# Optimization experiments

Measured on AMD Instinct MI355X. Metric: run time of the kernel, lower is better.

The kernel has to match this reference:

```python
import jax, jax.numpy as jnp
import numpy as np

IN_C, OUT_C, SCALE, S, NF = 2, 2, 2, 3, 64
MODES = 3
NB = IN_C * MODES  # one sub-module per (input channel, mode)
PAD = S - 1


def _pixel_shuffle(x, r):
    n, c, h, w = x.shape
    oc = c // (r * r)
    x = x.reshape(n, oc, r, r, h, w).transpose(0, 1, 4, 2, 5, 3)
    return x.reshape(n, oc, h * r, w * r)


def _round_ste(x):
    # straight-through round: forward = round(x), backward = identity
    return x + jax.lax.stop_gradient(jnp.round(x) - x)


def _branch(xin, w1, b1, w2, b2, w3, b3, w4, b4, w5, b5, w6, b6):
    # xin: [4B, 2, H+PAD, W+PAD]; tiny SxS conv then dense 1x1 chain (MuLUT unit)
    y = jax.lax.conv_general_dilated(xin, w1, (1, 1), 'VALID',
                                     dimension_numbers=('NCHW', 'OIHW', 'NCHW'))
    y = jax.nn.relu(y + b1[None, :, None, None])

    def dense(t, w, b):
        f = jax.nn.relu(jnp.einsum('bchw,oc->bohw', t, w) + b[None, :, None, None])
        return jnp.concatenate([t, f], axis=1)

    y = dense(y, w2, b2)
    y = dense(y, w3, b3)
    y = dense(y, w4, b4)
    y = dense(y, w5, b5)
    return jnp.einsum('bchw,oc->bohw', y, w6) + b6[None, :, None, None]


def _forward(x, prev_x, W1, B1, W2, B2, W3, B3, W4, B4, W5, B5, W6, B6):
    B, _, H, W = x.shape

    def prep(c):
        # rotating x and prev_x jointly == rotating each separately (elementwise pairing preserved)
        xc = jnp.concatenate([x[:, c:c + 1], prev_x[:, c:c + 1]], axis=1)  # [B,2,H,W]
        rs = jnp.concatenate([jnp.rot90(xc, k=r, axes=(2, 3)) for r in range(4)], axis=0)  # [4B,2,H,W]
        return jnp.pad(rs, ((0, 0), (0, 0), (0, PAD), (0, PAD)), mode='edge')  # replicate pad right/bottom

    xs = jnp.stack([prep(c) for c in range(IN_C)])           # [IN_C,4B,2,Hp,Wp]
    xb = xs[np.repeat(np.arange(IN_C), MODES)]               # [NB,4B,2,Hp,Wp]
    y = jax.vmap(_branch)(xb, W1, B1, W2, B2, W3, B3, W4, B4, W5, B5, W6, B6)  # [NB,4B,OC*sc^2,H,W]
    y = jax.vmap(lambda t: _pixel_shuffle(t, SCALE))(y)      # [NB,4B,OC,sH,sW]
    y = y.reshape(NB, 4, B, OUT_C, SCALE * H, SCALE * W)
    y = jnp.stack([jnp.rot90(y[:, r], k=(4 - r) % 4, axes=(3, 4)) for r in range(4)], axis=1)
    y = _round_ste(jnp.tanh(y) * 127.0)
    # sum over rotations and modes per channel, then over channels; divide by in_c (output_quant=False)
    return y.sum(axis=(0, 1)) / IN_C


def setup_inputs():
    key = jax.random.key(0)
    ks = jax.random.split(key, 8)
    B, H = 2, 64

    def w(k, shape, fan_in):
        return jax.random.normal(k, shape, jnp.float32) * np.float32(np.sqrt(2.0 / fan_in))

    return {
        'x': jax.random.uniform(ks[0], (B, IN_C, H, H), jnp.float32),
        'prev_x': jax.random.uniform(ks[1], (B, IN_C, H, H), jnp.float32),
        'W1': w(ks[2], (NB, NF, 2, S, S), 2 * S * S), 'B1': jnp.zeros((NB, NF), jnp.float32),
        'W2': w(ks[3], (NB, NF, NF), NF), 'B2': jnp.zeros((NB, NF), jnp.float32),
        'W3': w(ks[4], (NB, NF, 2 * NF), 2 * NF), 'B3': jnp.zeros((NB, NF), jnp.float32),
        'W4': w(ks[5], (NB, NF, 3 * NF), 3 * NF), 'B4': jnp.zeros((NB, NF), jnp.float32),
        'W5': w(ks[6], (NB, NF, 4 * NF), 4 * NF), 'B5': jnp.zeros((NB, NF), jnp.float32),
        'W6': w(ks[7], (NB, OUT_C * SCALE * SCALE, 5 * NF), 5 * NF),
        'B6': jnp.zeros((NB, OUT_C * SCALE * SCALE), jnp.float32),
    }


def reference(x, prev_x, W1, B1, W2, B2, W3, B3, W4, B4, W5, B5, W6, B6):
    return _forward(x, prev_x, W1, B1, W2, B2, W3, B3, W4, B4, W5, B5, W6, B6)
```

## Files before the change

### kernel.cpp

```cpp
#include <hip/hip_runtime.h>
#include <math.h>


typedef short bf16x8 __attribute__((ext_vector_type(8)));
typedef short short4v __attribute__((ext_vector_type(4)));
typedef float f32x4  __attribute__((ext_vector_type(4)));

__device__ __forceinline__ short f2bf_bits(float v) {
    union { float f; unsigned u; } x; x.f = v;
    unsigned r = x.u + 0x7FFFu + ((x.u >> 16) & 1u);
    return (short)(r >> 16);
}
__device__ __forceinline__ float bf2f(short s) {
    union { unsigned u; float f; } x; x.u = ((unsigned)(unsigned short)s) << 16;
    return x.f;
}

__global__ void prep_weights(const float* __restrict__ W1, const float* __restrict__ W2,
                             const float* __restrict__ W3, const float* __restrict__ W4,
                             const float* __restrict__ W5, const float* __restrict__ W6,
                             short* __restrict__ wsw, float* __restrict__ w1p,
                             float* __restrict__ outz)
{
    if (blockIdx.x < 135) {
        const int t = blockIdx.x * 256 + threadIdx.x;
        const int frag = t >> 6, lane = t & 63;
        const int b = frag / 90, slot = frag % 90;
        const int kqh = lane >> 4, rowl = lane & 15;
        const float* src; int K, kb, m; bool head = false;
        if (slot < 8)       { src = W2; K = 64;  kb = slot >> 2;        m = slot & 3; }
        else if (slot < 24) { src = W3; K = 128; kb = (slot - 8) >> 2;  m = slot & 3; }
        else if (slot < 48) { src = W4; K = 192; kb = (slot - 24) >> 2; m = slot & 3; }
        else if (slot < 80) { src = W5; K = 256; kb = (slot - 48) >> 2; m = slot & 3; }
        else                { src = W6; K = 320; kb = slot - 80; m = 0; head = true; }
        short* hi = wsw + (size_t)b * 92160 + slot * 1024 + (lane << 3);
        short* lo = hi + 512;
        #pragma unroll
        for (int j = 0; j < 8; ++j) {
            const int k = kb * 32 + ((j & 4) ? 16 : 0) + kqh * 4 + (j & 3);
            float v;
            if (!head) v = src[(size_t)(b * 64 + m * 16 + rowl) * K + k];
            else       v = (rowl < 8) ? src[(size_t)(b * 8 + rowl) * 320 + k] : 0.0f;
            const short h = f2bf_bits(v);
            hi[j] = h;
            lo[j] = f2bf_bits(v - bf2f(h));
        }
    } else if (blockIdx.x == 135) {
        for (int d = threadIdx.x; d < 6912; d += 256) {
            const int bq = d / 288, rem = d % 288;
            const int it2 = rem >> 4, s16 = (rem >> 2) & 3, tt = rem & 3;
            const int b = bq >> 2, kq = bq & 3;
            const int img = it2 / 9, tap = it2 % 9;
            w1p[d] = W1[(size_t)((b * 64 + s16 * 16 + kq * 4 + tt) * 2 + img) * 9 + tap];
        }
    } else {
        const int i = ((blockIdx.x - 136) * 256 + (int)threadIdx.x) * 8;
        f32x4 z = {0.f, 0.f, 0.f, 0.f};
        *(f32x4*)(outz + i)     = z;
        *(f32x4*)(outz + i + 4) = z;
    }
}

__device__ __forceinline__ void pack_kb(const f32x4 a, const f32x4 bq,
                                        bf16x8* ph, bf16x8* pl) {
    bf16x8 h, l;
    #pragma unroll
    for (int e = 0; e < 4; ++e) {
        float v = fmaxf(a[e], 0.0f);
        short hs = f2bf_bits(v);
        h[e] = hs; l[e] = f2bf_bits(v - bf2f(hs));
        float v2 = fmaxf(bq[e], 0.0f);
        short hs2 = f2bf_bits(v2);
        h[4 + e] = hs2; l[4 + e] = f2bf_bits(v2 - bf2f(hs2));
    }
    *ph = h; *pl = l;
}

__device__ __forceinline__ float sel4(int kq, const float* __restrict__ p) {
    const float b0 = p[0], b1 = p[4], b2 = p[8], b3 = p[12];
    const float lo = (kq & 1) ? b1 : b0;
    const float hi = (kq & 1) ? b3 : b2;
    return (kq & 2) ? hi : lo;
}

#define ASM_VMCNT(N) asm volatile("s_waitcnt vmcnt(" #N ")" ::: "memory")

#define DENSE_STAGE(KB_IN, SLOT0, BPTR, OUTKB)                                          \
  {                                                                                      \
    f32x4 sacc[4];                                                                       \
    _Pragma("unroll") for (int m = 0; m < 4; ++m)                                        \
      _Pragma("unroll") for (int rr = 0; rr < 4; ++rr) sacc[m][rr] = 0.f;                \
    _Pragma("unroll") for (int kb = 0; kb < KB_IN; ++kb) {                               \
      _Pragma("unroll") for (int m = 0; m < 4; ++m) {                                    \
        const int so = (SLOT0 + kb * 4 + m) * 1024 + lane8;                              \
        bf16x8 ah = *(const bf16x8*)&wlds[so];                                           \
        bf16x8 al = *(const bf16x8*)&wlds[so + 512];                                     \
        sacc[m] = __builtin_amdgcn_mfma_f32_16x16x32_bf16(ah, act_h[kb], sacc[m], 0, 0, 0); \
        sacc[m] = __builtin_amdgcn_mfma_f32_16x16x32_bf16(ah, act_l[kb], sacc[m], 0, 0, 0); \
        sacc[m] = __builtin_amdgcn_mfma_f32_16x16x32_bf16(al, act_h[kb], sacc[m], 0, 0, 0); \
      }                                                                                  \
    }                                                                                    \
    _Pragma("unroll") for (int m = 0; m < 4; ++m)                                        \
      _Pragma("unroll") for (int rr = 0; rr < 4; ++rr)                                   \
        sacc[m][rr] += sel4(kq, BPTR + m * 16 + rr);                                     \
    pack_kb(sacc[0], sacc[1], &act_h[OUTKB], &act_l[OUTKB]);                             \
    pack_kb(sacc[2], sacc[3], &act_h[OUTKB + 1], &act_l[OUTKB + 1]);                     \
  }

__global__ __launch_bounds__(1024) void mulut_main(
    const float* __restrict__ x, const float* __restrict__ px_,
    const float* __restrict__ B1, const float* __restrict__ B2,
    const float* __restrict__ B3, const float* __restrict__ B4,
    const float* __restrict__ B5, const float* __restrict__ B6,
    const short* __restrict__ wsw, const float* __restrict__ w1p,
    float* __restrict__ out)
{
    __shared__ short wlds[81920];

    const int blk = blockIdx.x;
    const int q   = blk & 15;
    const int n   = (blk >> 4) & 7;
    const int b   = blk >> 7;
    const int c   = (b >= 3) ? 1 : 0;
    const int r   = n >> 1;
    const int batch = n & 1;

    const int tid   = threadIdx.x;
    const int w     = tid >> 6;
    const int lane  = tid & 63;
    const int col   = lane & 15;
    const int kq    = lane >> 4;
    const int lane8 = lane << 3;

    const int row = q * 4 + (w >> 2);
    const int px  = (w & 3) * 16 + col;

    const char* wsb = (const char*)(wsw + (size_t)b * 92160);

    bf16x8 act_h[10];
    bf16x8 act_l[10];

    {
        const float* img0 = x   + ((batch * 2 + c) << 12);
        const float* img1 = px_ + ((batch * 2 + c) << 12);
        float g[2][9];
        #pragma unroll
        for (int di = 0; di < 3; ++di) {
            const int ii = min(row + di, 63);
            #pragma unroll
            for (int dj = 0; dj < 3; ++dj) {
                const int jj = min(px + dj, 63);
                int si, sj;
                if      (r == 0) { si = ii;      sj = jj;      }
                else if (r == 1) { si = jj;      sj = 63 - ii; }
                else if (r == 2) { si = 63 - ii; sj = 63 - jj; }
                else             { si = 63 - jj; sj = ii;      }
                g[0][di * 3 + dj] = img0[si * 64 + sj];
                g[1][di * 3 + dj] = img1[si * 64 + sj];
            }
        }

        f32x4 accc[4];
        #pragma unroll
        for (int s16 = 0; s16 < 4; ++s16)
            #pragma unroll
            for (int t = 0; t < 4; ++t) accc[s16][t] = 0.f;

        const f32x4* wp0 = (const f32x4*)&w1p[(b * 4 + kq) * 288];
        #pragma unroll
        for (int it = 0; it < 18; ++it) {
            const float gv = g[it / 9][it % 9];
            #pragma unroll
            for (int s16 = 0; s16 < 4; ++s16) {
                const f32x4 w4 = wp0[it * 4 + s16];
                #pragma unroll
                for (int t = 0; t < 4; ++t)
                    accc[s16][t] = fmaf(gv, w4[t], accc[s16][t]);
            }
        }
        #pragma unroll
        for (int m = 0; m < 4; ++m)
            #pragma unroll
            for (int rr = 0; rr < 4; ++rr)
                accc[m][rr] += sel4(kq, B1 + b * 64 + m * 16 + rr);
        pack_kb(accc[0], accc[1], &act_h[0], &act_l[0]);
        pack_kb(accc[2], accc[3], &act_h[1], &act_l[1]);
    }

    __builtin_amdgcn_sched_barrier(0);

    #pragma unroll
    for (int ck = 0; ck < 10; ++ck) {
        const unsigned off = ck * 16384 + w * 1024;
        __builtin_amdgcn_global_load_lds((const unsigned*)(wsb + off + lane * 16),
                                         (unsigned*)&wlds[off >> 1], 16, 0, 0);
    }
    __builtin_amdgcn_sched_barrier(0);

    ASM_VMCNT(9);
    __builtin_amdgcn_s_barrier();
    DENSE_STAGE(2, 0, B2 + b * 64, 2)

    ASM_VMCNT(7);
    __builtin_amdgcn_s_barrier();
    DENSE_STAGE(4, 8, B3 + b * 64, 4)

    __builtin_amdgcn_s_barrier();
    {
        const unsigned l0 = w * 1024;
        __builtin_amdgcn_global_load_lds((const unsigned*)(wsb + 163840 + l0 + lane * 16),
                                         (unsigned*)&wlds[l0 >> 1], 16, 0, 0);
        const unsigned l1 = 16384 + w * 256;
        __builtin_amdgcn_global_load_lds((const unsigned*)(wsb + 163840 + l1 + lane * 4),
                                         (unsigned*)&wlds[l1 >> 1], 4, 0, 0);
    }
    __builtin_amdgcn_sched_barrier(0);

    ASM_VMCNT(6);
    __builtin_amdgcn_s_barrier();
    DENSE_STAGE(6, 24, B4 + b * 64, 6)

    ASM_VMCNT(2);
    __builtin_amdgcn_s_barrier();
    DENSE_STAGE(8, 48, B5 + b * 64, 8)

    ASM_VMCNT(0);
    __builtin_amdgcn_s_barrier();

    f32x4 hacc;
    #pragma unroll
    for (int rr = 0; rr < 4; ++rr) hacc[rr] = 0.f;
    #pragma unroll
    for (int kb = 0; kb < 10; ++kb) {
        const int so = kb * 1024 + lane8;
        bf16x8 ah = *(const bf16x8*)&wlds[so];
        bf16x8 al = *(const bf16x8*)&wlds[so + 512];
        hacc = __builtin_amdgcn_mfma_f32_16x16x32_bf16(ah, act_h[kb], hacc, 0, 0, 0);
        hacc = __builtin_amdgcn_mfma_f32_16x16x32_bf16(ah, act_l[kb], hacc, 0, 0, 0);
        hacc = __builtin_amdgcn_mfma_f32_16x16x32_bf16(al, act_h[kb], hacc, 0, 0, 0);
    }
    #pragma unroll
    for (int rr = 0; rr < 4; ++rr) {
        const float h0 = B6[b * 8 + rr];
        const float h1 = B6[b * 8 + 4 + rr];
        hacc[rr] += (kq == 0) ? h0 : ((kq == 1) ? h1 : 0.f);
    }

    #pragma unroll
    for (int rr = 0; rr < 4; ++rr) {
        const int ch = kq * 4 + rr;
        if (ch < 8) {
            const int oc = ch >> 2;
            const int a  = (ch >> 1) & 1;
            const int bb = ch & 1;
            const int ip = 2 * row + a;
            const int jp = 2 * px + bb;
            int I, J;
            if      (r == 0) { I = ip;       J = jp;       }
            else if (r == 1) { I = jp;       J = 127 - ip; }
            else if (r == 2) { I = 127 - ip; J = 127 - jp; }
            else             { I = 127 - jp; J = ip;       }
            const float v = rintf(tanhf(hacc[rr]) * 127.0f);
            atomicAdd(out + (((batch * 2 + oc) << 14) + I * 128 + J), v * 0.5f);
        }
    }
}

extern "C" void kernel_launch(void* const* d_in, const int* in_sizes, int n_in,
                              void* d_out, int out_size, void* d_ws, size_t ws_size,
                              hipStream_t stream) {
    const float* x   = (const float*)d_in[0];
    const float* pxv = (const float*)d_in[1];
    const float* W1  = (const float*)d_in[2];
    const float* B1  = (const float*)d_in[3];
    const float* W2  = (const float*)d_in[4];
    const float* B2  = (const float*)d_in[5];
    const float* W3  = (const float*)d_in[6];
    const float* B3  = (const float*)d_in[7];
    const float* W4  = (const float*)d_in[8];
    const float* B4  = (const float*)d_in[9];
    const float* W5  = (const float*)d_in[10];
    const float* B5  = (const float*)d_in[11];
    const float* W6  = (const float*)d_in[12];
    const float* B6  = (const float*)d_in[13];
    float* out = (float*)d_out;

    short* wsw = (short*)d_ws;
    float* w1p = (float*)(wsw + 6 * 92160);

    prep_weights<<<dim3(168), dim3(256), 0, stream>>>(W1, W2, W3, W4, W5, W6,
                                                      wsw, w1p, out);
    mulut_main<<<dim3(768), dim3(1024), 0, stream>>>(
        x, pxv, B1, B2, B3, B4, B5, B6, wsw, w1p, out);
}
```

Baseline: 206.3 us.

## Double-buffer weight slots in smaller LDS, halve block size, stage weight prep via shared memory

The main kernel now uses 512-thread blocks with two rows per strip and a 64KB LDS split into two ping-pong buffers. Weight chunks stream in per stage and overlap with the MFMA work, which lets up to four blocks share a CU instead of one 160KB block. The prep kernel loads each weight matrix into shared memory with coalesced reads before swizzling, and writes vectorised bf16 hi/lo fragments using a padded per-branch stride. In exchange there are more barriers and more blocks, and each weight byte is reloaded from L2 by twice as many blocks.

```diff
diff --git a/kernel.cpp b/kernel.cpp
--- a/kernel.cpp
+++ b/kernel.cpp
@@ -3,8 +3,8 @@
 
 
 typedef short bf16x8 __attribute__((ext_vector_type(8)));
-typedef short short4v __attribute__((ext_vector_type(4)));
 typedef float f32x4  __attribute__((ext_vector_type(4)));
+typedef float f32x4g __attribute__((ext_vector_type(4)));
 
 __device__ __forceinline__ short f2bf_bits(float v) {
     union { float f; unsigned u; } x; x.f = v;
@@ -22,31 +22,49 @@
                              short* __restrict__ wsw, float* __restrict__ w1p,
                              float* __restrict__ outz)
 {
-    if (blockIdx.x < 135) {
-        const int t = blockIdx.x * 256 + threadIdx.x;
-        const int frag = t >> 6, lane = t & 63;
-        const int b = frag / 90, slot = frag % 90;
-        const int kqh = lane >> 4, rowl = lane & 15;
-        const float* src; int K, kb, m; bool head = false;
-        if (slot < 8)       { src = W2; K = 64;  kb = slot >> 2;        m = slot & 3; }
-        else if (slot < 24) { src = W3; K = 128; kb = (slot - 8) >> 2;  m = slot & 3; }
-        else if (slot < 48) { src = W4; K = 192; kb = (slot - 24) >> 2; m = slot & 3; }
-        else if (slot < 80) { src = W5; K = 256; kb = (slot - 48) >> 2; m = slot & 3; }
-        else                { src = W6; K = 320; kb = slot - 80; m = 0; head = true; }
-        short* hi = wsw + (size_t)b * 92160 + slot * 1024 + (lane << 3);
-        short* lo = hi + 512;
-        #pragma unroll
-        for (int j = 0; j < 8; ++j) {
-            const int k = kb * 32 + ((j & 4) ? 16 : 0) + kqh * 4 + (j & 3);
-            float v;
-            if (!head) v = src[(size_t)(b * 64 + m * 16 + rowl) * K + k];
-            else       v = (rowl < 8) ? src[(size_t)(b * 8 + rowl) * 320 + k] : 0.0f;
-            const short h = f2bf_bits(v);
-            hi[j] = h;
-            lo[j] = f2bf_bits(v - bf2f(h));
-        }
-    } else if (blockIdx.x == 135) {
-        for (int d = threadIdx.x; d < 6912; d += 256) {
+    __shared__ float S[16384];
+    const int blk = blockIdx.x, tid = threadIdx.x;
+
+    if (blk < 30) {
+        const int b = blk / 5, s = blk % 5;
+        const float* Wsrc[5] = { W2, W3, W4, W5, W6 };
+        const int rows = (s < 4) ? 64 : 8;
+        const int K    = 64 * (s + 1);
+        const int N    = rows * K;
+        const int slotbase[5] = { 0, 8, 24, 48, 80 };
+        const int nslots[5]   = { 8, 16, 24, 32, 12 };
+
+        const float* src = Wsrc[s] + (size_t)b * N;
+        for (int i = tid; i < (N >> 2); i += 256)
+            *(f32x4g*)&S[i << 2] = *(const f32x4g*)&src[i << 2];
+        __syncthreads();
+
+        const int NS = nslots[s];
+        for (int pp = tid; pp < NS * 64; pp += 256) {
+            const int l    = pp >> 6;
+            const int lane = pp & 63;
+            const int kb   = (s < 4) ? (l >> 2) : l;
+            const int m    = (s < 4) ? (l & 3) : 0;
+            const int rowl = lane & 15;
+            const int kqh  = lane >> 4;
+            bf16x8 hv, lv;
+            #pragma unroll
+            for (int j = 0; j < 8; ++j) {
+                const int k = kb * 32 + ((j & 4) ? 16 : 0) + kqh * 4 + (j & 3);
+                float v;
+                if (s < 4)                    v = S[(m * 16 + rowl) * K + k];
+                else if (rowl < 8 && l < 10)  v = S[rowl * 320 + k];
+                else                          v = 0.0f;
+                const short h = f2bf_bits(v);
+                hv[j] = h;
+                lv[j] = f2bf_bits(v - bf2f(h));
+            }
+            short* dst = wsw + (size_t)b * 94208 + (slotbase[s] + l) * 1024 + (lane << 3);
+            *(bf16x8*)dst         = hv;
+            *(bf16x8*)(dst + 512) = lv;
+        }
+    } else if (blk == 30) {
+        for (int d = tid; d < 6912; d += 256) {
             const int bq = d / 288, rem = d % 288;
             const int it2 = rem >> 4, s16 = (rem >> 2) & 3, tt = rem & 3;
             const int b = bq >> 2, kq = bq & 3;
@@ -54,10 +72,10 @@
             w1p[d] = W1[(size_t)((b * 64 + s16 * 16 + kq * 4 + tt) * 2 + img) * 9 + tap];
         }
     } else {
-        const int i = ((blockIdx.x - 136) * 256 + (int)threadIdx.x) * 8;
-        f32x4 z = {0.f, 0.f, 0.f, 0.f};
-        *(f32x4*)(outz + i)     = z;
-        *(f32x4*)(outz + i + 4) = z;
+        const int i = ((blk - 31) * 256 + tid) * 8;
+        f32x4g z = {0.f, 0.f, 0.f, 0.f};
+        *(f32x4g*)(outz + i)     = z;
+        *(f32x4g*)(outz + i + 4) = z;
     }
 }
 
@@ -84,30 +102,39 @@
 }
 
 #define ASM_VMCNT(N) asm volatile("s_waitcnt vmcnt(" #N ")" ::: "memory")
-
-#define DENSE_STAGE(KB_IN, SLOT0, BPTR, OUTKB)                                          \
-  {                                                                                      \
-    f32x4 sacc[4];                                                                       \
-    _Pragma("unroll") for (int m = 0; m < 4; ++m)                                        \
-      _Pragma("unroll") for (int rr = 0; rr < 4; ++rr) sacc[m][rr] = 0.f;                \
-    _Pragma("unroll") for (int kb = 0; kb < KB_IN; ++kb) {                               \
-      _Pragma("unroll") for (int m = 0; m < 4; ++m) {                                    \
-        const int so = (SLOT0 + kb * 4 + m) * 1024 + lane8;                              \
-        bf16x8 ah = *(const bf16x8*)&wlds[so];                                           \
-        bf16x8 al = *(const bf16x8*)&wlds[so + 512];                                     \
-        sacc[m] = __builtin_amdgcn_mfma_f32_16x16x32_bf16(ah, act_h[kb], sacc[m], 0, 0, 0); \
-        sacc[m] = __builtin_amdgcn_mfma_f32_16x16x32_bf16(ah, act_l[kb], sacc[m], 0, 0, 0); \
-        sacc[m] = __builtin_amdgcn_mfma_f32_16x16x32_bf16(al, act_h[kb], sacc[m], 0, 0, 0); \
-      }                                                                                  \
-    }                                                                                    \
-    _Pragma("unroll") for (int m = 0; m < 4; ++m)                                        \
-      _Pragma("unroll") for (int rr = 0; rr < 4; ++rr)                                   \
-        sacc[m][rr] += sel4(kq, BPTR + m * 16 + rr);                                     \
-    pack_kb(sacc[0], sacc[1], &act_h[OUTKB], &act_l[OUTKB]);                             \
-    pack_kb(sacc[2], sacc[3], &act_h[OUTKB + 1], &act_l[OUTKB + 1]);                     \
+#define MFMA(A, B, C) __builtin_amdgcn_mfma_f32_16x16x32_bf16(A, B, C, 0, 0, 0)
+
+#define ISSUE(SLOT0, NC, PB)                                                          \
+  _Pragma("unroll") for (int c = 0; c < NC; ++c) {                                    \
+    const unsigned lo_ = c * 8192u + w * 1024u;                                       \
+    __builtin_amdgcn_global_load_lds(                                                 \
+        (const unsigned*)(wsb + (SLOT0) * 2048 + lo_ + lane * 16),                    \
+        (unsigned*)&wlds[(PB) + (lo_ >> 1)], 16, 0, 0);                               \
   }
 
-__global__ __launch_bounds__(1024) void mulut_main(
+#define HALF(SACC, NKB, A0, PB, SLOT0)                                                \
+  _Pragma("unroll") for (int kb = 0; kb < NKB; ++kb)                                  \
+    _Pragma("unroll") for (int m = 0; m < 4; ++m) {                                   \
+      const int so = (PB) + ((SLOT0) + kb * 4 + m) * 1024 + lane8;                    \
+      bf16x8 ah = *(const bf16x8*)&wlds[so];                                          \
+      bf16x8 al = *(const bf16x8*)&wlds[so + 512];                                    \
+      SACC[m] = MFMA(ah, act_h[(A0) + kb], SACC[m]);                                  \
+      SACC[m] = MFMA(ah, act_l[(A0) + kb], SACC[m]);                                  \
+      SACC[m] = MFMA(al, act_h[(A0) + kb], SACC[m]);                                  \
+    }
+
+#define SACC_INIT(SACC)                                                               \
+  _Pragma("unroll") for (int m = 0; m < 4; ++m)                                       \
+    _Pragma("unroll") for (int rr = 0; rr < 4; ++rr) SACC[m][rr] = 0.f;
+
+#define FINISH(SACC, BPTR, OUTKB)                                                     \
+  _Pragma("unroll") for (int m = 0; m < 4; ++m)                                       \
+    _Pragma("unroll") for (int rr = 0; rr < 4; ++rr)                                  \
+      SACC[m][rr] += sel4(kq, (BPTR) + m * 16 + rr);                                  \
+  pack_kb(SACC[0], SACC[1], &act_h[OUTKB], &act_l[OUTKB]);                            \
+  pack_kb(SACC[2], SACC[3], &act_h[(OUTKB) + 1], &act_l[(OUTKB) + 1]);
+
+__global__ __launch_bounds__(512, 4) void mulut_main(
     const float* __restrict__ x, const float* __restrict__ px_,
     const float* __restrict__ B1, const float* __restrict__ B2,
     const float* __restrict__ B3, const float* __restrict__ B4,
@@ -115,14 +142,15 @@
     const short* __restrict__ wsw, const float* __restrict__ w1p,
     float* __restrict__ out)
 {
-    __shared__ short wlds[81920];
-
-    const int blk = blockIdx.x;
-    const int q   = blk & 15;
-    const int n   = (blk >> 4) & 7;
-    const int b   = blk >> 7;
-    const int c   = (b >= 3) ? 1 : 0;
-    const int r   = n >> 1;
+    __shared__ short wlds[32768];
+    const int P1 = 16384;
+
+    const int blk   = blockIdx.x;
+    const int strip = blk & 31;
+    const int n     = (blk >> 5) & 7;
+    const int b     = blk >> 8;
+    const int c     = (b >= 3) ? 1 : 0;
+    const int r     = n >> 1;
     const int batch = n & 1;
 
     const int tid   = threadIdx.x;
@@ -132,10 +160,10 @@
     const int kq    = lane >> 4;
     const int lane8 = lane << 3;
 
-    const int row = q * 4 + (w >> 2);
+    const int row = strip * 2 + (w >> 2);
     const int px  = (w & 3) * 16 + col;
 
-    const char* wsb = (const char*)(wsw + (size_t)b * 92160);
+    const char* wsb = (const char*)(wsw + (size_t)b * 94208);
 
     bf16x8 act_h[10];
     bf16x8 act_l[10];
@@ -159,13 +187,8 @@
                 g[1][di * 3 + dj] = img1[si * 64 + sj];
             }
         }
-
         f32x4 accc[4];
-        #pragma unroll
-        for (int s16 = 0; s16 < 4; ++s16)
-            #pragma unroll
-            for (int t = 0; t < 4; ++t) accc[s16][t] = 0.f;
-
+        SACC_INIT(accc)
         const f32x4* wp0 = (const f32x4*)&w1p[(b * 4 + kq) * 288];
         #pragma unroll
         for (int it = 0; it < 18; ++it) {
@@ -178,51 +201,66 @@
                     accc[s16][t] = fmaf(gv, w4[t], accc[s16][t]);
             }
         }
-        #pragma unroll
-        for (int m = 0; m < 4; ++m)
-            #pragma unroll
-            for (int rr = 0; rr < 4; ++rr)
-                accc[m][rr] += sel4(kq, B1 + b * 64 + m * 16 + rr);
-        pack_kb(accc[0], accc[1], &act_h[0], &act_l[0]);
-        pack_kb(accc[2], accc[3], &act_h[1], &act_l[1]);
-    }
-
-    __builtin_amdgcn_sched_barrier(0);
-
-    #pragma unroll
-    for (int ck = 0; ck < 10; ++ck) {
-        const unsigned off = ck * 16384 + w * 1024;
-        __builtin_amdgcn_global_load_lds((const unsigned*)(wsb + off + lane * 16),
-                                         (unsigned*)&wlds[off >> 1], 16, 0, 0);
-    }
-    __builtin_amdgcn_sched_barrier(0);
-
-    ASM_VMCNT(9);
-    __builtin_amdgcn_s_barrier();
-    DENSE_STAGE(2, 0, B2 + b * 64, 2)
-
-    ASM_VMCNT(7);
-    __builtin_amdgcn_s_barrier();
-    DENSE_STAGE(4, 8, B3 + b * 64, 4)
-
-    __builtin_amdgcn_s_barrier();
-    {
-        const unsigned l0 = w * 1024;
-        __builtin_amdgcn_global_load_lds((const unsigned*)(wsb + 163840 + l0 + lane * 16),
-                                         (unsigned*)&wlds[l0 >> 1], 16, 0, 0);
-        const unsigned l1 = 16384 + w * 256;
-        __builtin_amdgcn_global_load_lds((const unsigned*)(wsb + 163840 + l1 + lane * 4),
-                                         (unsigned*)&wlds[l1 >> 1], 4, 0, 0);
-    }
-    __builtin_amdgcn_sched_barrier(0);
-
-    ASM_VMCNT(6);
-    __builtin_amdgcn_s_barrier();
-    DENSE_STAGE(6, 24, B4 + b * 64, 6)
-
-    ASM_VMCNT(2);
-    __builtin_amdgcn_s_barrier();
-    DENSE_STAGE(8, 48, B5 + b * 64, 8)
+        FINISH(accc, B1 + b * 64, 0)
+    }
+
+    __builtin_amdgcn_sched_barrier(0);
+    ISSUE(0, 4, 0)
+    ISSUE(16, 4, P1)
+    __builtin_amdgcn_sched_barrier(0);
+
+    ASM_VMCNT(4);
+    __builtin_amdgcn_s_barrier();
+
+    f32x4 sacc[4];
+    SACC_INIT(sacc)
+    HALF(sacc, 2, 0, 0, 0)
+    FINISH(sacc, B2 + b * 64, 2)
+    f32x4 sacc2[4];
+    SACC_INIT(sacc2)
+    HALF(sacc2, 2, 0, 0, 8)
+
+    __builtin_amdgcn_s_barrier();
+    __builtin_amdgcn_sched_barrier(0);
+    ISSUE(32, 4, 0)
+    __builtin_amdgcn_sched_barrier(0);
+    ASM_VMCNT(4);
+    __builtin_amdgcn_s_barrier();
+
+    HALF(sacc2, 2, 2, P1, 0)
+    FINISH(sacc2, B3 + b * 64, 4)
+    SACC_INIT(sacc)
+    HALF(sacc, 2, 0, P1, 8)
+
+    __builtin_amdgcn_s_barrier();
+    __builtin_amdgcn_sched_barrier(0);
+    ISSUE(48, 4, P1)
+    __builtin_amdgcn_sched_barrier(0);
+    ASM_VMCNT(4);
+    __builtin_amdgcn_s_barrier();
+
+    HALF(sacc, 4, 2, 0, 0)
+    FINISH(sacc, B4 + b * 64, 6)
+
+    __builtin_amdgcn_s_barrier();
+    __builtin_amdgcn_sched_barrier(0);
+    ISSUE(64, 4, 0)
+    __builtin_amdgcn_sched_barrier(0);
+    ASM_VMCNT(4);
+    __builtin_amdgcn_s_barrier();
+
+    SACC_INIT(sacc)
+    HALF(sacc, 4, 0, P1, 0)
+
+    __builtin_amdgcn_s_barrier();
+    __builtin_amdgcn_sched_barrier(0);
+    ISSUE(80, 3, P1)
+    __builtin_amdgcn_sched_barrier(0);
+    ASM_VMCNT(3);
+    __builtin_amdgcn_s_barrier();
+
+    HALF(sacc, 4, 4, 0, 0)
+    FINISH(sacc, B5 + b * 64, 8)
 
     ASM_VMCNT(0);
     __builtin_amdgcn_s_barrier();
@@ -232,12 +270,12 @@
     for (int rr = 0; rr < 4; ++rr) hacc[rr] = 0.f;
     #pragma unroll
     for (int kb = 0; kb < 10; ++kb) {
-        const int so = kb * 1024 + lane8;
+        const int so = P1 + kb * 1024 + lane8;
         bf16x8 ah = *(const bf16x8*)&wlds[so];
         bf16x8 al = *(const bf16x8*)&wlds[so + 512];
-        hacc = __builtin_amdgcn_mfma_f32_16x16x32_bf16(ah, act_h[kb], hacc, 0, 0, 0);
-        hacc = __builtin_amdgcn_mfma_f32_16x16x32_bf16(ah, act_l[kb], hacc, 0, 0, 0);
-        hacc = __builtin_amdgcn_mfma_f32_16x16x32_bf16(al, act_h[kb], hacc, 0, 0, 0);
+        hacc = MFMA(ah, act_h[kb], hacc);
+        hacc = MFMA(ah, act_l[kb], hacc);
+        hacc = MFMA(al, act_h[kb], hacc);
     }
     #pragma unroll
     for (int rr = 0; rr < 4; ++rr) {
@@ -286,10 +324,10 @@
     float* out = (float*)d_out;
 
     short* wsw = (short*)d_ws;
-    float* w1p = (float*)(wsw + 6 * 92160);
-
-    prep_weights<<<dim3(168), dim3(256), 0, stream>>>(W1, W2, W3, W4, W5, W6,
-                                                      wsw, w1p, out);
-    mulut_main<<<dim3(768), dim3(1024), 0, stream>>>(
+    float* w1p = (float*)(wsw + 6 * 94208);
+
+    prep_weights<<<dim3(63), dim3(256), 0, stream>>>(W1, W2, W3, W4, W5, W6,
+                                                     wsw, w1p, out);
+    mulut_main<<<dim3(1536), dim3(512), 0, stream>>>(
         x, pxv, B1, B2, B3, B4, B5, B6, wsw, w1p, out);
 }
```

New measurement: 180.0 us. 1.15x faster.
